# Performance work log

Measured on AMD Instinct MI355X. Metric: run time of the kernel, lower is better.

## Reference

```python
import jax, jax.numpy as jnp
import numpy as np

A, B, M, H, MAX_NB, N_MOLS = 100000, 200000, 20000, 256, 10, 2000
ATOM_FDIM, BOND_FDIM, DEPTH = 35, 5, 3


def setup_inputs() -> dict:
    key = jax.random.key(0)
    ks = jax.random.split(key, 10)
    fatoms = jax.random.normal(ks[0], (A, ATOM_FDIM), dtype=jnp.float32)
    fbonds = jax.random.normal(ks[1], (B, ATOM_FDIM + BOND_FDIM), dtype=jnp.float32)
    agraph = jax.random.randint(ks[2], (A, MAX_NB), 0, M + B)
    bgraph = jax.random.randint(ks[3], (B, MAX_NB), 0, M + B)
    tree_message = jax.random.normal(ks[4], (M, H), dtype=jnp.float32)
    tree_message = tree_message.at[0].set(0.0)  # all_mess[0] is the zero pad vector
    atom_scope = jnp.sort(jax.random.randint(ks[5], (A,), 0, N_MOLS))
    s = 1.0 / np.sqrt(H)
    W_i = jax.random.normal(ks[6], (ATOM_FDIM + BOND_FDIM, H), dtype=jnp.float32) * s
    W_h = jax.random.normal(ks[7], (H, H), dtype=jnp.float32) * s
    W_o_w = jax.random.normal(ks[8], (ATOM_FDIM + H, H), dtype=jnp.float32) * s
    W_o_b = jax.random.normal(ks[9], (H,), dtype=jnp.float32) * s
    return {"fatoms": fatoms, "fbonds": fbonds, "agraph": agraph, "bgraph": bgraph,
            "tree_message": tree_message, "atom_scope": atom_scope,
            "W_i": W_i, "W_h": W_h, "W_o_w": W_o_w, "W_o_b": W_o_b}


def reference(fatoms, fbonds, agraph, bgraph, tree_message, atom_scope, W_i, W_h, W_o_w, W_o_b):
    binput = fbonds @ W_i                       # [B, H]
    graph_message = jax.nn.relu(binput)
    for _ in range(DEPTH - 1):
        message = jnp.concatenate([tree_message, graph_message], axis=0)  # [M+B, H]
        nei = message[bgraph].sum(axis=1)       # gather [B, MAX_NB, H] -> sum -> [B, H]
        graph_message = jax.nn.relu(binput + nei @ W_h)
    message = jnp.concatenate([tree_message, graph_message], axis=0)
    nei = message[agraph].sum(axis=1)           # [A, H]
    ainput = jnp.concatenate([fatoms, nei], axis=1)  # [A, ATOM_FDIM + H]
    atom_hiddens = jax.nn.relu(ainput @ W_o_w + W_o_b)
    # scope-based segment-mean pooling over atoms of each molecule
    sums = jax.ops.segment_sum(atom_hiddens, atom_scope, num_segments=N_MOLS)
    counts = jax.ops.segment_sum(jnp.ones((atom_hiddens.shape[0],), atom_hiddens.dtype),
                                 atom_scope, num_segments=N_MOLS)
    return sums / jnp.maximum(counts, 1.0)[:, None]
```

## Files before the change

### kernel.cpp

```cpp
#include <hip/hip_runtime.h>
#include <cstdint>
#include <cstddef>

#define A_N 100000
#define B_N 200000
#define M_N 20000
#define POOL_N 220000
#define HD 256
#define MAX_NB 10
#define N_MOLS 2000
#define ATOM_FDIM 35
#define FB_DIM 40

typedef unsigned short u16;
typedef __attribute__((ext_vector_type(8))) short bf16x8;
typedef __attribute__((ext_vector_type(4))) float f32x4;

__device__ u16 g_msg0[(size_t)B_N * HD];
__device__ u16 g_msg1[(size_t)B_N * HD];
__device__ u16 g_tmsgh[(size_t)M_N * HD];
__device__ u16 g_P[(size_t)POOL_N * HD];
__device__ u16 g_Q[(size_t)POOL_N * HD];
__device__ u16 g_binH[(size_t)B_N * HD];
__device__ u16 g_Fh[(size_t)A_N * HD];
__device__ u16 g_pWh_hi[65536], g_pWh_lo[65536];
__device__ u16 g_pWo_hi[65536], g_pWo_lo[65536];
__device__ float g_counts[N_MOLS];

__device__ __forceinline__ u16 f2b(float f)
{
    union { float f; unsigned u; } x; x.f = f;
    const unsigned r = x.u + 0x7FFFu + ((x.u >> 16) & 1u);
    return (u16)(r >> 16);
}
__device__ __forceinline__ float b2f(u16 h) { return __uint_as_float((unsigned)h << 16); }
__device__ __forceinline__ float blo(unsigned u) { return __uint_as_float(u << 16); }
__device__ __forceinline__ float bhi(unsigned u) { return __uint_as_float(u & 0xffff0000u); }

__device__ __forceinline__ int lbound(const int* __restrict__ s, int n, int v)
{
    int l = 0, r = n;
    while (l < r) { const int mid = (l + r) >> 1; if (s[mid] < v) l = mid + 1; else r = mid; }
    return l;
}

__global__ __launch_bounds__(256)
void k_setup(float* __restrict__ out, const float* __restrict__ tmsg,
             const float* __restrict__ Wh, const float* __restrict__ Wo,
             const int* __restrict__ scope)
{
    const int bid = blockIdx.x;
    const int tid = threadIdx.x;
    if (bid < 2000) {
        out[bid * 256 + tid] = 0.f;
    } else if (bid < 7000) {
        const int i = ((bid - 2000) * 256 + tid) * 4;
        if (i < M_N * HD) {
            const float4 v = *(const float4*)(tmsg + i);
            ushort4 o;
            o.x = f2b(v.x); o.y = f2b(v.y); o.z = f2b(v.z); o.w = f2b(v.w);
            *(ushort4*)(g_tmsgh + i) = o;
        }
    } else if (bid < 7032) {
        const int id = (bid - 7000) * 256 + tid;
        const int l = id & 63;
        const int t = (id >> 6) & 15;
        const int c = id >> 10;
        const int n = t * 16 + (l & 15);
        const int kb = c * 32 + ((l >> 4) << 3);
        const size_t base = (size_t)id * 8;
        #pragma unroll
        for (int j = 0; j < 8; ++j) {
            const int k = kb + j;
            const float wh = Wh[(size_t)k * HD + n];
            const u16 hh = f2b(wh);
            g_pWh_hi[base + j] = hh;
            g_pWh_lo[base + j] = f2b(wh - b2f(hh));
            const float wo = Wo[(size_t)(35 + k) * HD + n];
            const u16 oh = f2b(wo);
            g_pWo_hi[base + j] = oh;
            g_pWo_lo[base + j] = f2b(wo - b2f(oh));
        }
    } else {
        const int m = (bid - 7032) * 256 + tid;
        if (m < N_MOLS) {
            const int lo = lbound(scope, A_N, m);
            const int hi = lbound(scope, A_N, m + 1);
            g_counts[m] = (float)(hi - lo);
        }
    }
}

__global__ __launch_bounds__(256, 2)
void k_in(const float* __restrict__ fbonds, const float* __restrict__ Wi)
{
    const int lane = threadIdx.x & 63;
    const int wid  = (blockIdx.x * 256 + threadIdx.x) >> 6;
    const int nw   = (gridDim.x * 256) >> 6;

    float4 w[FB_DIM];
    #pragma unroll
    for (int k = 0; k < FB_DIM; ++k)
        w[k] = *(const float4*)&Wi[(size_t)k * HD + lane * 4];

    #pragma unroll 1
    for (int row = wid; row < B_N; row += nw) {
        const float* fr = fbonds + (size_t)row * FB_DIM;
        float ax = 0.f, ay = 0.f, az = 0.f, aw = 0.f;
        #pragma unroll
        for (int q = 0; q < FB_DIM / 4; ++q) {
            const float4 fv = *(const float4*)(fr + q * 4);
            ax += fv.x * w[q*4+0].x; ay += fv.x * w[q*4+0].y;
            az += fv.x * w[q*4+0].z; aw += fv.x * w[q*4+0].w;
            ax += fv.y * w[q*4+1].x; ay += fv.y * w[q*4+1].y;
            az += fv.y * w[q*4+1].z; aw += fv.y * w[q*4+1].w;
            ax += fv.z * w[q*4+2].x; ay += fv.z * w[q*4+2].y;
            az += fv.z * w[q*4+2].z; aw += fv.z * w[q*4+2].w;
            ax += fv.w * w[q*4+3].x; ay += fv.w * w[q*4+3].y;
            az += fv.w * w[q*4+3].z; aw += fv.w * w[q*4+3].w;
        }
        const size_t base = (size_t)row * HD + lane * 4;
        ushort4 bi;
        bi.x = f2b(ax); bi.y = f2b(ay); bi.z = f2b(az); bi.w = f2b(aw);
        *(ushort4*)(g_binH + base) = bi;
        ushort4 o;
        o.x = f2b(fmaxf(ax, 0.f)); o.y = f2b(fmaxf(ay, 0.f));
        o.z = f2b(fmaxf(az, 0.f)); o.w = f2b(fmaxf(aw, 0.f));
        *(ushort4*)(g_msg0 + base) = o;
    }
}

__global__ __launch_bounds__(256, 2)
void k_gemmMF(int sel, int rowStart, int rowEnd)
{
    const u16* msrc = (sel == 1) ? g_msg1 : g_msg0;
    const u16* pHi  = (sel == 2) ? g_pWo_hi : g_pWh_hi;
    const u16* pLo  = (sel == 2) ? g_pWo_lo : g_pWh_lo;
    u16* dst        = (sel == 2) ? g_Q : g_P;

    const int tid  = threadIdx.x;
    const int lane = tid & 63;
    const int wv   = tid >> 6;
    const int l15  = lane & 15;
    const int quad = lane >> 4;
    const int tOff = (wv & 1) * 8;

    int rowIdeal[4];
    const u16* srow[4];
    #pragma unroll
    for (int rg = 0; rg < 4; ++rg) {
        const int ri = rowStart + blockIdx.x * 128 + (wv >> 1) * 64 + rg * 16 + l15;
        rowIdeal[rg] = ri;
        const int r = (ri < rowEnd) ? ri : (rowEnd - 1);
        srow[rg] = (r < M_N) ? (g_tmsgh + (size_t)r * HD)
                             : (msrc + (size_t)(r - M_N) * HD);
    }

    f32x4 acc[4][8];
    #pragma unroll
    for (int rg = 0; rg < 4; ++rg)
        #pragma unroll
        for (int t = 0; t < 8; ++t)
            acc[rg][t] = (f32x4){0.f, 0.f, 0.f, 0.f};

    bf16x8 b0 = *(const bf16x8*)(srow[0] + quad * 8);
    bf16x8 b1 = *(const bf16x8*)(srow[1] + quad * 8);
    bf16x8 b2 = *(const bf16x8*)(srow[2] + quad * 8);
    bf16x8 b3 = *(const bf16x8*)(srow[3] + quad * 8);

    #pragma unroll 1
    for (int c = 0; c < 8; ++c) {
        const int cn = (c + 1) & 7;
        const bf16x8 n0 = *(const bf16x8*)(srow[0] + cn * 32 + quad * 8);
        const bf16x8 n1 = *(const bf16x8*)(srow[1] + cn * 32 + quad * 8);
        const bf16x8 n2 = *(const bf16x8*)(srow[2] + cn * 32 + quad * 8);
        const bf16x8 n3 = *(const bf16x8*)(srow[3] + cn * 32 + quad * 8);
        const u16* ph = pHi + ((size_t)(c * 16 + tOff) * 64 + lane) * 8;
        const u16* pl = pLo + ((size_t)(c * 16 + tOff) * 64 + lane) * 8;
        #pragma unroll
        for (int t = 0; t < 8; ++t) {
            const bf16x8 ah = *(const bf16x8*)(ph + (size_t)t * 512);
            acc[0][t] = __builtin_amdgcn_mfma_f32_16x16x32_bf16(ah, b0, acc[0][t], 0, 0, 0);
            acc[1][t] = __builtin_amdgcn_mfma_f32_16x16x32_bf16(ah, b1, acc[1][t], 0, 0, 0);
            acc[2][t] = __builtin_amdgcn_mfma_f32_16x16x32_bf16(ah, b2, acc[2][t], 0, 0, 0);
            acc[3][t] = __builtin_amdgcn_mfma_f32_16x16x32_bf16(ah, b3, acc[3][t], 0, 0, 0);
            const bf16x8 al = *(const bf16x8*)(pl + (size_t)t * 512);
            acc[0][t] = __builtin_amdgcn_mfma_f32_16x16x32_bf16(al, b0, acc[0][t], 0, 0, 0);
            acc[1][t] = __builtin_amdgcn_mfma_f32_16x16x32_bf16(al, b1, acc[1][t], 0, 0, 0);
            acc[2][t] = __builtin_amdgcn_mfma_f32_16x16x32_bf16(al, b2, acc[2][t], 0, 0, 0);
            acc[3][t] = __builtin_amdgcn_mfma_f32_16x16x32_bf16(al, b3, acc[3][t], 0, 0, 0);
        }
        b0 = n0; b1 = n1; b2 = n2; b3 = n3;
    }

    #pragma unroll
    for (int rg = 0; rg < 4; ++rg) {
        if (rowIdeal[rg] < rowEnd) {
            u16* drow = dst + (size_t)rowIdeal[rg] * HD + tOff * 16 + quad * 4;
            #pragma unroll
            for (int t = 0; t < 8; ++t) {
                ushort4 o;
                o.x = f2b(acc[rg][t][0]); o.y = f2b(acc[rg][t][1]);
                o.z = f2b(acc[rg][t][2]); o.w = f2b(acc[rg][t][3]);
                *(ushort4*)(drow + t * 16) = o;
            }
        }
    }
}

__global__ __launch_bounds__(256)
void k_gather(const int* __restrict__ bgraph, int dstSel, int rowOff)
{
    u16* dst = dstSel ? g_msg1 : g_msg0;
    __shared__ int idx_s[8][MAX_NB];
    const int tid = threadIdx.x;
    const int rowBase = rowOff + blockIdx.x * 8;
    if (tid < 8 * MAX_NB) {
        const int r = tid / MAX_NB;
        const int j = tid - r * MAX_NB;
        idx_s[r][j] = bgraph[(size_t)(rowBase + r) * MAX_NB + j];
    }
    __syncthreads();
    const int rl = tid >> 5;
    const int c  = (tid & 31) << 3;
    const int row = rowBase + rl;

    const uint4 bv = *(const uint4*)(g_binH + (size_t)row * HD + c);
    float s[8] = {0.f,0.f,0.f,0.f,0.f,0.f,0.f,0.f};
    #pragma unroll
    for (int j = 0; j < MAX_NB; ++j) {
        const uint4 v = *(const uint4*)(g_P + (size_t)idx_s[rl][j] * HD + c);
        s[0] += blo(v.x); s[1] += bhi(v.x);
        s[2] += blo(v.y); s[3] += bhi(v.y);
        s[4] += blo(v.z); s[5] += bhi(v.z);
        s[6] += blo(v.w); s[7] += bhi(v.w);
    }
    uint4 w;
    w.x = ((unsigned)f2b(fmaxf(s[0] + blo(bv.x), 0.f)))
        | ((unsigned)f2b(fmaxf(s[1] + bhi(bv.x), 0.f)) << 16);
    w.y = ((unsigned)f2b(fmaxf(s[2] + blo(bv.y), 0.f)))
        | ((unsigned)f2b(fmaxf(s[3] + bhi(bv.y), 0.f)) << 16);
    w.z = ((unsigned)f2b(fmaxf(s[4] + blo(bv.z), 0.f)))
        | ((unsigned)f2b(fmaxf(s[5] + bhi(bv.z), 0.f)) << 16);
    w.w = ((unsigned)f2b(fmaxf(s[6] + blo(bv.w), 0.f)))
        | ((unsigned)f2b(fmaxf(s[7] + bhi(bv.w), 0.f)) << 16);
    *(uint4*)(dst + (size_t)row * HD + c) = w;
}

__global__ __launch_bounds__(256, 2)
void k_F(const float* __restrict__ fatoms, const float* __restrict__ Wo,
         const float* __restrict__ bias)
{
    const int lane = threadIdx.x & 63;
    const int wid  = (blockIdx.x * 256 + threadIdx.x) >> 6;
    const int nw   = (gridDim.x * 256) >> 6;

    float4 w[ATOM_FDIM];
    #pragma unroll
    for (int k = 0; k < ATOM_FDIM; ++k)
        w[k] = *(const float4*)&Wo[(size_t)k * HD + lane * 4];
    const float4 b4 = *(const float4*)&bias[lane * 4];

    #pragma unroll 1
    for (int row = wid; row < A_N; row += nw) {
        const float* fr = fatoms + (size_t)row * ATOM_FDIM;
        float ax = b4.x, ay = b4.y, az = b4.z, aw = b4.w;
        #pragma unroll
        for (int k = 0; k < ATOM_FDIM; ++k) {
            const float f = fr[k];
            ax += f * w[k].x; ay += f * w[k].y;
            az += f * w[k].z; aw += f * w[k].w;
        }
        ushort4 o;
        o.x = f2b(ax); o.y = f2b(ay); o.z = f2b(az); o.w = f2b(aw);
        *(ushort4*)(g_Fh + (size_t)row * HD + lane * 4) = o;
    }
}

__global__ __launch_bounds__(256)
void k_gatherA(const int* __restrict__ agraph, const int* __restrict__ scope,
               float* __restrict__ out)
{
    __shared__ int idx_s[64 * MAX_NB];
    __shared__ int sc_s[64];
    const int tid = threadIdx.x;
    const int rb = blockIdx.x * 64;
    for (int i = tid; i < 64 * MAX_NB; i += 256) {
        const int a = rb + i / MAX_NB;
        idx_s[i] = (a < A_N) ? agraph[(size_t)a * MAX_NB + (i % MAX_NB)] : 0;
    }
    if (tid < 64) sc_s[tid] = (rb + tid < A_N) ? scope[rb + tid] : -1;
    __syncthreads();

    const int grp = tid >> 5;
    const int c = (tid & 31) * 8;
    float s[8] = {0.f,0.f,0.f,0.f,0.f,0.f,0.f,0.f};
    int prev = -1;
    #pragma unroll 1
    for (int i = 0; i < 8; ++i) {
        const int al = grp * 8 + i;
        const int a = rb + al;
        if (a < A_N) {
            const int m = sc_s[al];
            if (m != prev) {
                if (prev >= 0) {
                    float* dst = out + (size_t)prev * HD + c;
                    #pragma unroll
                    for (int q = 0; q < 8; ++q) atomicAdd(dst + q, s[q]);
                    #pragma unroll
                    for (int q = 0; q < 8; ++q) s[q] = 0.f;
                }
                prev = m;
            }
            const uint4 fv = *(const uint4*)(g_Fh + (size_t)a * HD + c);
            float g0=0.f,g1=0.f,g2=0.f,g3=0.f,g4=0.f,g5=0.f,g6=0.f,g7=0.f;
            #pragma unroll
            for (int j = 0; j < MAX_NB; ++j) {
                const uint4 v = *(const uint4*)(g_Q + (size_t)idx_s[al * MAX_NB + j] * HD + c);
                g0 += blo(v.x); g1 += bhi(v.x);
                g2 += blo(v.y); g3 += bhi(v.y);
                g4 += blo(v.z); g5 += bhi(v.z);
                g6 += blo(v.w); g7 += bhi(v.w);
            }
            s[0] += fmaxf(g0 + blo(fv.x), 0.f); s[1] += fmaxf(g1 + bhi(fv.x), 0.f);
            s[2] += fmaxf(g2 + blo(fv.y), 0.f); s[3] += fmaxf(g3 + bhi(fv.y), 0.f);
            s[4] += fmaxf(g4 + blo(fv.z), 0.f); s[5] += fmaxf(g5 + bhi(fv.z), 0.f);
            s[6] += fmaxf(g6 + blo(fv.w), 0.f); s[7] += fmaxf(g7 + bhi(fv.w), 0.f);
        }
    }
    if (prev >= 0) {
        float* dst = out + (size_t)prev * HD + c;
        #pragma unroll
        for (int q = 0; q < 8; ++q) atomicAdd(dst + q, s[q]);
    }
}

__global__ __launch_bounds__(256)
void k_div(float* __restrict__ out)
{
    const int idx = blockIdx.x * 256 + threadIdx.x;
    out[idx] = out[idx] / fmaxf(g_counts[idx >> 8], 1.0f);
}

extern "C" void kernel_launch(void* const* d_in, const int* in_sizes, int n_in,
                              void* d_out, int out_size, void* d_ws, size_t ws_size,
                              hipStream_t stream)
{
    const float* fatoms = (const float*)d_in[0];
    const float* fbonds = (const float*)d_in[1];
    const int*   agraph = (const int*)d_in[2];
    const int*   bgraph = (const int*)d_in[3];
    const float* tmsg   = (const float*)d_in[4];
    const int*   scope  = (const int*)d_in[5];
    const float* W_i    = (const float*)d_in[6];
    const float* W_h    = (const float*)d_in[7];
    const float* W_o    = (const float*)d_in[8];
    const float* W_ob   = (const float*)d_in[9];
    float* out = (float*)d_out;

    (void)d_ws; (void)ws_size;

    k_setup<<<7040, 256, 0, stream>>>(out, tmsg, W_h, W_o, scope);
    k_in<<<512, 256, 0, stream>>>(fbonds, W_i);

    k_gemmMF<<<(POOL_N + 127) / 128, 256, 0, stream>>>(0, 0, POOL_N);
    for (int ch = 0; ch < 4; ++ch)
        k_gather<<<B_N / 32, 256, 0, stream>>>(bgraph, 1, ch * (B_N / 4));
    k_gemmMF<<<(B_N + 127) / 128, 256, 0, stream>>>(1, M_N, POOL_N);
    for (int ch = 0; ch < 4; ++ch)
        k_gather<<<B_N / 32, 256, 0, stream>>>(bgraph, 0, ch * (B_N / 4));

    k_gemmMF<<<(POOL_N + 127) / 128, 256, 0, stream>>>(2, 0, POOL_N);
    k_F<<<512, 256, 0, stream>>>(fatoms, W_o, W_ob);
    k_gatherA<<<(A_N + 63) / 64, 256, 0, stream>>>(agraph, scope, out);
    k_div<<<(N_MOLS * HD) / 256, 256, 0, stream>>>(out);
}
```

Baseline: 1.288 ms.

## Pool atoms per molecule via segment starts, dropping atomics and divide kernel

Setup now computes molecule start offsets by binary search instead of counts, and no longer zeroes the output. The atom gather kernel assigns two blocks per molecule (one per half of the hidden dimension), sums its atoms' relu outputs, reduces through shared memory and writes the mean directly. This removes the global float atomics, the output zeroing and the separate divide launch. In exchange, the per-molecule atom counts vary, so load balance across blocks is uneven, and each block's 16-way reduction over atoms is sequential.

```diff
diff --git a/kernel.cpp b/kernel.cpp
--- a/kernel.cpp
+++ b/kernel.cpp
@@ -25,7 +25,7 @@
 __device__ u16 g_Fh[(size_t)A_N * HD];
 __device__ u16 g_pWh_hi[65536], g_pWh_lo[65536];
 __device__ u16 g_pWo_hi[65536], g_pWo_lo[65536];
-__device__ float g_counts[N_MOLS];
+__device__ int g_mstart[N_MOLS + 1];
 
 __device__ __forceinline__ u16 f2b(float f)
 {
@@ -45,24 +45,22 @@
 }
 
 __global__ __launch_bounds__(256)
-void k_setup(float* __restrict__ out, const float* __restrict__ tmsg,
+void k_setup(const float* __restrict__ tmsg,
              const float* __restrict__ Wh, const float* __restrict__ Wo,
              const int* __restrict__ scope)
 {
     const int bid = blockIdx.x;
     const int tid = threadIdx.x;
-    if (bid < 2000) {
-        out[bid * 256 + tid] = 0.f;
-    } else if (bid < 7000) {
-        const int i = ((bid - 2000) * 256 + tid) * 4;
+    if (bid < 5000) {
+        const int i = (bid * 256 + tid) * 4;
         if (i < M_N * HD) {
             const float4 v = *(const float4*)(tmsg + i);
             ushort4 o;
             o.x = f2b(v.x); o.y = f2b(v.y); o.z = f2b(v.z); o.w = f2b(v.w);
             *(ushort4*)(g_tmsgh + i) = o;
         }
-    } else if (bid < 7032) {
-        const int id = (bid - 7000) * 256 + tid;
+    } else if (bid < 5032) {
+        const int id = (bid - 5000) * 256 + tid;
         const int l = id & 63;
         const int t = (id >> 6) & 15;
         const int c = id >> 10;
@@ -82,12 +80,8 @@
             g_pWo_lo[base + j] = f2b(wo - b2f(oh));
         }
     } else {
-        const int m = (bid - 7032) * 256 + tid;
-        if (m < N_MOLS) {
-            const int lo = lbound(scope, A_N, m);
-            const int hi = lbound(scope, A_N, m + 1);
-            g_counts[m] = (float)(hi - lo);
-        }
+        const int m = (bid - 5032) * 256 + tid;
+        if (m <= N_MOLS) g_mstart[m] = lbound(scope, A_N, m);
     }
 }
 
@@ -278,68 +272,52 @@
 }
 
 __global__ __launch_bounds__(256)
-void k_gatherA(const int* __restrict__ agraph, const int* __restrict__ scope,
-               float* __restrict__ out)
-{
-    __shared__ int idx_s[64 * MAX_NB];
-    __shared__ int sc_s[64];
+void k_gatherA(const int* __restrict__ agraph, float* __restrict__ out)
+{
+    const int mol = blockIdx.x >> 1;
+    const int ch  = (blockIdx.x & 1) * 128;
     const int tid = threadIdx.x;
-    const int rb = blockIdx.x * 64;
-    for (int i = tid; i < 64 * MAX_NB; i += 256) {
-        const int a = rb + i / MAX_NB;
-        idx_s[i] = (a < A_N) ? agraph[(size_t)a * MAX_NB + (i % MAX_NB)] : 0;
-    }
-    if (tid < 64) sc_s[tid] = (rb + tid < A_N) ? scope[rb + tid] : -1;
+    const int grp = tid >> 4;
+    const int lc  = (tid & 15) * 8;
+    const int c   = ch + lc;
+
+    const int s0 = g_mstart[mol];
+    const int s1 = g_mstart[mol + 1];
+
+    float s[8] = {0.f,0.f,0.f,0.f,0.f,0.f,0.f,0.f};
+    #pragma unroll 1
+    for (int a = s0 + grp; a < s1; a += 16) {
+        const int* ap = agraph + (size_t)a * MAX_NB;
+        int idx[MAX_NB];
+        #pragma unroll
+        for (int j = 0; j < MAX_NB; ++j) idx[j] = ap[j];
+        const uint4 fv = *(const uint4*)(g_Fh + (size_t)a * HD + c);
+        float g0=0.f,g1=0.f,g2=0.f,g3=0.f,g4=0.f,g5=0.f,g6=0.f,g7=0.f;
+        #pragma unroll
+        for (int j = 0; j < MAX_NB; ++j) {
+            const uint4 v = *(const uint4*)(g_Q + (size_t)idx[j] * HD + c);
+            g0 += blo(v.x); g1 += bhi(v.x);
+            g2 += blo(v.y); g3 += bhi(v.y);
+            g4 += blo(v.z); g5 += bhi(v.z);
+            g6 += blo(v.w); g7 += bhi(v.w);
+        }
+        s[0] += fmaxf(g0 + blo(fv.x), 0.f); s[1] += fmaxf(g1 + bhi(fv.x), 0.f);
+        s[2] += fmaxf(g2 + blo(fv.y), 0.f); s[3] += fmaxf(g3 + bhi(fv.y), 0.f);
+        s[4] += fmaxf(g4 + blo(fv.z), 0.f); s[5] += fmaxf(g5 + bhi(fv.z), 0.f);
+        s[6] += fmaxf(g6 + blo(fv.w), 0.f); s[7] += fmaxf(g7 + bhi(fv.w), 0.f);
+    }
+
+    __shared__ float red[16][128];
+    #pragma unroll
+    for (int q = 0; q < 8; ++q) red[grp][lc + q] = s[q];
     __syncthreads();
-
-    const int grp = tid >> 5;
-    const int c = (tid & 31) * 8;
-    float s[8] = {0.f,0.f,0.f,0.f,0.f,0.f,0.f,0.f};
-    int prev = -1;
-    #pragma unroll 1
-    for (int i = 0; i < 8; ++i) {
-        const int al = grp * 8 + i;
-        const int a = rb + al;
-        if (a < A_N) {
-            const int m = sc_s[al];
-            if (m != prev) {
-                if (prev >= 0) {
-                    float* dst = out + (size_t)prev * HD + c;
-                    #pragma unroll
-                    for (int q = 0; q < 8; ++q) atomicAdd(dst + q, s[q]);
-                    #pragma unroll
-                    for (int q = 0; q < 8; ++q) s[q] = 0.f;
-                }
-                prev = m;
-            }
-            const uint4 fv = *(const uint4*)(g_Fh + (size_t)a * HD + c);
-            float g0=0.f,g1=0.f,g2=0.f,g3=0.f,g4=0.f,g5=0.f,g6=0.f,g7=0.f;
-            #pragma unroll
-            for (int j = 0; j < MAX_NB; ++j) {
-                const uint4 v = *(const uint4*)(g_Q + (size_t)idx_s[al * MAX_NB + j] * HD + c);
-                g0 += blo(v.x); g1 += bhi(v.x);
-                g2 += blo(v.y); g3 += bhi(v.y);
-                g4 += blo(v.z); g5 += bhi(v.z);
-                g6 += blo(v.w); g7 += bhi(v.w);
-            }
-            s[0] += fmaxf(g0 + blo(fv.x), 0.f); s[1] += fmaxf(g1 + bhi(fv.x), 0.f);
-            s[2] += fmaxf(g2 + blo(fv.y), 0.f); s[3] += fmaxf(g3 + bhi(fv.y), 0.f);
-            s[4] += fmaxf(g4 + blo(fv.z), 0.f); s[5] += fmaxf(g5 + bhi(fv.z), 0.f);
-            s[6] += fmaxf(g6 + blo(fv.w), 0.f); s[7] += fmaxf(g7 + bhi(fv.w), 0.f);
-        }
-    }
-    if (prev >= 0) {
-        float* dst = out + (size_t)prev * HD + c;
-        #pragma unroll
-        for (int q = 0; q < 8; ++q) atomicAdd(dst + q, s[q]);
-    }
-}
-
-__global__ __launch_bounds__(256)
-void k_div(float* __restrict__ out)
-{
-    const int idx = blockIdx.x * 256 + threadIdx.x;
-    out[idx] = out[idx] / fmaxf(g_counts[idx >> 8], 1.0f);
+    if (tid < 128) {
+        float acc = 0.f;
+        #pragma unroll
+        for (int g = 0; g < 16; ++g) acc += red[g][tid];
+        const float inv = 1.0f / fmaxf((float)(s1 - s0), 1.0f);
+        out[(size_t)mol * HD + ch + tid] = acc * inv;
+    }
 }
 
 extern "C" void kernel_launch(void* const* d_in, const int* in_sizes, int n_in,
@@ -360,7 +338,7 @@
 
     (void)d_ws; (void)ws_size;
 
-    k_setup<<<7040, 256, 0, stream>>>(out, tmsg, W_h, W_o, scope);
+    k_setup<<<5040, 256, 0, stream>>>(tmsg, W_h, W_o, scope);
     k_in<<<512, 256, 0, stream>>>(fbonds, W_i);
 
     k_gemmMF<<<(POOL_N + 127) / 128, 256, 0, stream>>>(0, 0, POOL_N);
@@ -372,6 +350,5 @@
 
     k_gemmMF<<<(POOL_N + 127) / 128, 256, 0, stream>>>(2, 0, POOL_N);
     k_F<<<512, 256, 0, stream>>>(fatoms, W_o, W_ob);
-    k_gatherA<<<(A_N + 63) / 64, 256, 0, stream>>>(agraph, scope, out);
-    k_div<<<(N_MOLS * HD) / 256, 256, 0, stream>>>(out);
-}
+    k_gatherA<<<N_MOLS * 2, 256, 0, stream>>>(agraph, out);
+}
```

Measured after the change: 1.200 ms. -6.9%, faster.
